# Performance work log

Hardware: AMD Instinct MI355X
Metric: run time of the kernel (lower is better)

## Reference

```python
import jax, jax.numpy as jnp
import numpy as np

BN, S, D = 200, 128, 1024          # B*N entity rows, scenes, d_model
D_INNER, D_STATE, D_CONV = 2048, 32, 4


def setup_inputs() -> dict:
    key = jax.random.key(0)
    ks = jax.random.split(key, 8)
    s = 0.02
    return {
        "x": jax.random.normal(ks[0], (BN, S, D), jnp.float32),
        "emotion_bias": jax.random.uniform(ks[1], (BN, S, 1), jnp.float32),
        "norm_w": jnp.ones((D,), jnp.float32),
        "norm_b": jnp.zeros((D,), jnp.float32),
        "in_proj_W": jax.random.normal(ks[2], (2 * D_INNER, D), jnp.float32) * s,
        "conv_w": jax.random.normal(ks[3], (D_INNER, 1, D_CONV), jnp.float32) * 0.1,
        "conv_b": jnp.zeros((D_INNER,), jnp.float32),
        "x_proj_W": jax.random.normal(ks[4], (2 * D_STATE + 1, D_INNER), jnp.float32) * s,
        "dt_W": jax.random.normal(ks[5], (D_INNER, 1), jnp.float32),
        "dt_b": jnp.zeros((D_INNER,), jnp.float32),
        "out_W": jax.random.normal(ks[6], (D, D_INNER), jnp.float32) * s,
        "emotion_scale": jnp.array(0.1, jnp.float32),
    }


def reference(x, emotion_bias, norm_w, norm_b, in_proj_W, conv_w, conv_b,
              x_proj_W, dt_W, dt_b, out_W, emotion_scale):
    residual = x
    # LayerNorm (eps=1e-5, biased variance as in torch)
    mu = x.mean(-1, keepdims=True)
    var = ((x - mu) ** 2).mean(-1, keepdims=True)
    xn = (x - mu) * jax.lax.rsqrt(var + 1e-5) * norm_w + norm_b

    xz = xn @ in_proj_W.T                      # [BN, S, 2*d_inner]
    x_in, z = jnp.split(xz, 2, axis=-1)

    # causal depthwise conv1d (torch pads d_conv-1 both sides, truncates to S == left-pad only)
    xc = jax.lax.conv_general_dilated(
        x_in.transpose(0, 2, 1), conv_w,
        window_strides=(1,), padding=[(D_CONV - 1, 0)],
        feature_group_count=D_INNER,
        dimension_numbers=("NCH", "OIH", "NCH"))
    xc = (xc + conv_b[None, :, None]).transpose(0, 2, 1)   # [BN, S, d_inner]
    x_act = jax.nn.silu(xc)

    x_ssm = x_act @ x_proj_W.T                 # [BN, S, 2*d_state+1]
    delta_raw, B_mat, C = jnp.split(x_ssm, [1, 1 + D_STATE], axis=-1)
    delta = jax.nn.softplus(delta_raw @ dt_W.T + dt_b)     # [BN, S, d_inner]
    delta = jnp.maximum(delta + emotion_scale * emotion_bias, 1e-4)

    def step(h, inp):
        d_t, B_t, C_t, xa_t = inp              # [BN,d_inner],[BN,n],[BN,n],[BN,d_inner]
        h = h * jnp.exp(-d_t)[..., None] + B_t[:, None, :] * xa_t[..., None]
        h = jnp.clip(h, -100.0, 100.0)
        y_t = jnp.einsum("bdn,bn->bd", h, C_t)
        return h, y_t

    h0 = jnp.zeros((BN, D_INNER, D_STATE), jnp.float32)
    xs = (delta.transpose(1, 0, 2), B_mat.transpose(1, 0, 2),
          C.transpose(1, 0, 2), x_act.transpose(1, 0, 2))
    _, y = jax.lax.scan(step, h0, xs)          # y: [S, BN, d_inner]
    y = y.transpose(1, 0, 2)

    return (y * jax.nn.silu(z)) @ out_W.T + residual
```

## Files before the change

kernel.cpp:

```cpp
#include <hip/hip_runtime.h>
#include <cstdint>
#include <cstddef>

#define NBN   200
#define NS    128
#define ND    1024
#define NDI   2048
#define NST   32
#define NROWS (NBN * NS)

typedef __attribute__((ext_vector_type(8))) short bf16x8;
typedef __attribute__((ext_vector_type(4))) float f32x4;

__device__ __forceinline__ unsigned short f2bf(float f) {
    unsigned int u = __float_as_uint(f);
    u += 0x7fffu + ((u >> 16) & 1u);
    return (unsigned short)(u >> 16);
}
__device__ __forceinline__ float bf2f(unsigned short h) {
    return __uint_as_float(((unsigned int)h) << 16);
}

__device__ __forceinline__ void gl_lds16(const void* g, void* l) {
    typedef __attribute__((address_space(1))) const unsigned int* gp_t;
    typedef __attribute__((address_space(3))) unsigned int* lp_t;
    __builtin_amdgcn_global_load_lds((gp_t)(uintptr_t)g,
                                     (lp_t)(unsigned int)(uintptr_t)l, 16, 0, 0);
}

__global__ __launch_bounds__(256) void cvt_kernel(const float* __restrict__ src,
                                                  unsigned short* __restrict__ dst, int n) {
    int i = blockIdx.x * 256 + threadIdx.x;
    if (i < n) dst[i] = f2bf(src[i]);
}

__global__ __launch_bounds__(256) void padwx_kernel(const float* __restrict__ src,
                                                    unsigned short* __restrict__ dst) {
    int i = blockIdx.x * 256 + threadIdx.x;
    int r = i >> 11;
    dst[i] = (r < 65) ? f2bf(src[i]) : (unsigned short)0;
}

__global__ __launch_bounds__(256) void ln_kernel(const float* __restrict__ x,
                                                 const float* __restrict__ gw,
                                                 const float* __restrict__ gb,
                                                 unsigned short* __restrict__ xn) {
    __shared__ float ss[4], ss2[4];
    size_t row = blockIdx.x;
    int tid = threadIdx.x;
    const float4* px = (const float4*)(x + row * ND);
    float4 v = px[tid];
    float s  = v.x + v.y + v.z + v.w;
    float s2 = fmaf(v.x, v.x, fmaf(v.y, v.y, fmaf(v.z, v.z, v.w * v.w)));
    #pragma unroll
    for (int off = 32; off > 0; off >>= 1) {
        s  += __shfl_down(s,  off, 64);
        s2 += __shfl_down(s2, off, 64);
    }
    if ((tid & 63) == 0) { ss[tid >> 6] = s; ss2[tid >> 6] = s2; }
    __syncthreads();
    float tot  = ss[0] + ss[1] + ss[2] + ss[3];
    float tot2 = ss2[0] + ss2[1] + ss2[2] + ss2[3];
    float mu   = tot * (1.f / ND);
    float var  = fmaf(tot2, 1.f / ND, -mu * mu);
    float rstd = rsqrtf(var + 1e-5f);
    float4 wv = ((const float4*)gw)[tid];
    float4 bv = ((const float4*)gb)[tid];
    ushort4 o;
    o.x = f2bf(fmaf((v.x - mu) * rstd, wv.x, bv.x));
    o.y = f2bf(fmaf((v.y - mu) * rstd, wv.y, bv.y));
    o.z = f2bf(fmaf((v.z - mu) * rstd, wv.z, bv.z));
    o.w = f2bf(fmaf((v.w - mu) * rstd, wv.w, bv.w));
    ((ushort4*)(xn + row * ND))[tid] = o;
}

template <int EPI>
__global__ __launch_bounds__(256, 2)
void gemm_bt128(const unsigned short* __restrict__ A,
                const unsigned short* __restrict__ B,
                int K, int N,
                void* __restrict__ outp,
                const float* __restrict__ resid) {
    __shared__ __align__(16) unsigned short As[128 * 32];
    __shared__ __align__(16) unsigned short Bs[128 * 32];
    const int tid  = threadIdx.x;
    const int bm   = blockIdx.x;
    const int bn   = blockIdx.y;
    const int wid  = tid >> 6;
    const int lane = tid & 63;
    const int wm   = (wid >> 1) * 64;
    const int wn   = (wid & 1) * 64;
    const int lrow = lane & 15;
    const int kq   = lane >> 4;

    f32x4 acc[4][4];
    #pragma unroll
    for (int i = 0; i < 4; i++)
        #pragma unroll
        for (int j = 0; j < 4; j++) acc[i][j] = (f32x4){0.f, 0.f, 0.f, 0.f};

    const size_t a_row0 = (size_t)bm * 128;
    const size_t b_row0 = (size_t)bn * 128;

    const int r1 = tid >> 2;
    const int c8 = (tid & 3) << 3;
    const unsigned short* gA1 = A + (a_row0 + r1) * K + c8;
    const unsigned short* gA2 = A + (a_row0 + 64 + r1) * K + c8;
    const unsigned short* gB1 = B + (b_row0 + r1) * K + c8;
    const unsigned short* gB2 = B + (b_row0 + 64 + r1) * K + c8;
    char* lA1 = (char*)As + wid * 1024;
    char* lA2 = (char*)As + wid * 1024 + 4096;
    char* lB1 = (char*)Bs + wid * 1024;
    char* lB2 = (char*)Bs + wid * 1024 + 4096;

    for (int kt = 0; kt < K; kt += 32) {
        __syncthreads();
        gl_lds16(gA1, lA1); gl_lds16(gA2, lA2);
        gl_lds16(gB1, lB1); gl_lds16(gB2, lB2);
        gA1 += 32; gA2 += 32; gB1 += 32; gB2 += 32;
        __syncthreads();
        bf16x8 af[4], bfr[4];
        #pragma unroll
        for (int mi = 0; mi < 4; mi++)
            af[mi] = *(const bf16x8*)&As[(wm + mi * 16 + lrow) * 32 + kq * 8];
        #pragma unroll
        for (int ni = 0; ni < 4; ni++)
            bfr[ni] = *(const bf16x8*)&Bs[(wn + ni * 16 + lrow) * 32 + kq * 8];
        #pragma unroll
        for (int mi = 0; mi < 4; mi++)
            #pragma unroll
            for (int ni = 0; ni < 4; ni++)
                acc[mi][ni] = __builtin_amdgcn_mfma_f32_16x16x32_bf16(af[mi], bfr[ni], acc[mi][ni], 0, 0, 0);
    }

    #pragma unroll
    for (int mi = 0; mi < 4; mi++)
        #pragma unroll
        for (int ni = 0; ni < 4; ni++)
            #pragma unroll
            for (int r = 0; r < 4; r++) {
                size_t row = a_row0 + wm + mi * 16 + kq * 4 + r;
                size_t col = b_row0 + wn + ni * 16 + lrow;
                float v = acc[mi][ni][r];
                size_t idx = row * (size_t)N + col;
                if (EPI == 0) ((unsigned short*)outp)[idx] = f2bf(v);
                else          ((float*)outp)[idx] = v + resid[idx];
            }
}

__global__ __launch_bounds__(256) void conv_silu_kernel(const unsigned short* __restrict__ xz,
                                                        const float* __restrict__ cw,
                                                        const float* __restrict__ cb,
                                                        unsigned short* __restrict__ xact) {
    int tid = blockIdx.x * 256 + threadIdx.x;
    int c = tid & (NDI - 1);
    int b = tid >> 11;
    float4 wv = ((const float4*)cw)[c];
    float w0 = wv.x, w1 = wv.y, w2 = wv.z, w3 = wv.w;
    float bias = cb[c];
    const unsigned short* px = xz + (size_t)b * NS * (2 * NDI) + c;
    unsigned short* po = xact + (size_t)b * NS * NDI + c;
    float x0 = 0.f, x1 = 0.f, x2 = 0.f;
    for (int t = 0; t < NS; t++) {
        float x3 = bf2f(px[(size_t)t * (2 * NDI)]);
        float v  = fmaf(x3, w3, fmaf(x2, w2, fmaf(x1, w1, fmaf(x0, w0, bias))));
        float s  = v * __builtin_amdgcn_rcpf(1.f + __expf(-v));
        po[(size_t)t * NDI] = f2bf(s);
        x0 = x1; x1 = x2; x2 = x3;
    }
}

__global__ __launch_bounds__(256, 2)
void gemm2_kernel(const unsigned short* __restrict__ A,
                  const unsigned short* __restrict__ B,
                  float* __restrict__ out) {
    __shared__ __align__(16) unsigned short As[64 * 32];
    __shared__ __align__(16) unsigned short Bs[80 * 32];
    const int tid  = threadIdx.x;
    const int bm   = blockIdx.x;
    const int wid  = tid >> 6;
    const int lane = tid & 63;
    const int lrow = lane & 15;
    const int kq   = lane >> 4;

    f32x4 acc[5];
    #pragma unroll
    for (int i = 0; i < 5; i++) acc[i] = (f32x4){0.f, 0.f, 0.f, 0.f};

    const int r1 = tid >> 2;
    const int c8 = (tid & 3) << 3;
    const unsigned short* gA1 = A + ((size_t)bm * 64 + r1) * NDI + c8;
    const unsigned short* gB1 = B + (size_t)r1 * NDI + c8;
    const unsigned short* gB2 = B + (size_t)(64 + r1) * NDI + c8;
    char* lA1 = (char*)As + wid * 1024;
    char* lB1 = (char*)Bs + wid * 1024;
    char* lB2 = (char*)Bs + 4096;

    for (int kt = 0; kt < NDI; kt += 32) {
        __syncthreads();
        gl_lds16(gA1, lA1);
        gl_lds16(gB1, lB1);
        if (tid < 64) gl_lds16(gB2, lB2);
        gA1 += 32; gB1 += 32; gB2 += 32;
        __syncthreads();
        bf16x8 af = *(const bf16x8*)&As[(wid * 16 + lrow) * 32 + kq * 8];
        #pragma unroll
        for (int ni = 0; ni < 5; ni++) {
            bf16x8 bfr = *(const bf16x8*)&Bs[(ni * 16 + lrow) * 32 + kq * 8];
            acc[ni] = __builtin_amdgcn_mfma_f32_16x16x32_bf16(af, bfr, acc[ni], 0, 0, 0);
        }
    }
    #pragma unroll
    for (int ni = 0; ni < 5; ni++)
        #pragma unroll
        for (int r = 0; r < 4; r++) {
            size_t row = (size_t)bm * 64 + wid * 16 + kq * 4 + r;
            int col = ni * 16 + lrow;
            out[row * 80 + col] = acc[ni][r];
        }
}

__global__ __launch_bounds__(256)
void scan_kernel(const float* __restrict__ xssm,
                 unsigned short* xact_g,
                 const unsigned short* __restrict__ xz,
                 const float* __restrict__ dtW,
                 const float* __restrict__ dtb,
                 const float* __restrict__ eb,
                 const float* __restrict__ es_p) {
    __shared__ __align__(16) float sB[NS][NST];
    __shared__ __align__(16) float sC[NS][NST];
    __shared__ float sDR[NS];
    __shared__ float sDE[NS];
    const int tid = threadIdx.x;
    const int b   = blockIdx.y;
    const int d   = blockIdx.x * 256 + tid;

    for (int i = tid; i < NS * 65; i += 256) {
        int t = i / 65, c = i - t * 65;
        float v = xssm[((size_t)b * NS + t) * 80 + c];
        if (c == 0)      sDR[t] = v;
        else if (c < 33) sB[t][c - 1] = v;
        else             sC[t][c - 33] = v;
    }
    {
        float es = es_p[0];
        for (int i = tid; i < NS; i += 256) sDE[i] = es * eb[b * NS + i];
    }
    __syncthreads();

    const float w  = dtW[d];
    const float bb = dtb[d];
    float h[NST];
    #pragma unroll
    for (int n = 0; n < NST; n++) h[n] = 0.f;

    unsigned short* p        = xact_g + (size_t)b * NS * NDI + d;
    const unsigned short* pz = xz + (size_t)b * NS * (2 * NDI) + NDI + d;

    for (int t = 0; t < NS; t++) {
        float xa = bf2f(*p);
        float zz = bf2f(*pz);
        float raw = fmaf(sDR[t], w, bb);
        float sp  = (raw > 20.f) ? raw : __logf(1.f + __expf(raw));
        float delta = fmaxf(sp + sDE[t], 1e-4f);
        float a = __expf(-delta);
        float y = 0.f;
        #pragma unroll
        for (int n8 = 0; n8 < 8; n8++) {
            f32x4 Bv = *(const f32x4*)&sB[t][n8 * 4];
            f32x4 Cv = *(const f32x4*)&sC[t][n8 * 4];
            #pragma unroll
            for (int j = 0; j < 4; j++) {
                h[n8 * 4 + j] = fmaf(h[n8 * 4 + j], a, Bv[j] * xa);
                y = fmaf(h[n8 * 4 + j], Cv[j], y);
            }
        }
        float sig = __builtin_amdgcn_rcpf(1.f + __expf(-zz));
        *p = f2bf(y * zz * sig);
        p += NDI; pz += 2 * NDI;
    }
}

extern "C" void kernel_launch(void* const* d_in, const int* in_sizes, int n_in,
                              void* d_out, int out_size, void* d_ws, size_t ws_size,
                              hipStream_t stream) {
    const float* x   = (const float*)d_in[0];
    const float* eb  = (const float*)d_in[1];
    const float* nw  = (const float*)d_in[2];
    const float* nb  = (const float*)d_in[3];
    const float* Wi  = (const float*)d_in[4];
    const float* cw  = (const float*)d_in[5];
    const float* cb  = (const float*)d_in[6];
    const float* Wx  = (const float*)d_in[7];
    const float* dtW = (const float*)d_in[8];
    const float* dtb = (const float*)d_in[9];
    const float* Wo  = (const float*)d_in[10];
    const float* es  = (const float*)d_in[11];
    float* out = (float*)d_out;

    char* ws = (char*)d_ws;
    unsigned short* wi_b   = (unsigned short*)(ws + 0);
    unsigned short* wo_b   = (unsigned short*)(ws + 8388608);
    unsigned short* wx_b   = (unsigned short*)(ws + 12582912);
    unsigned short* xz_b   = (unsigned short*)(ws + 12910592);
    unsigned short* xact_b = (unsigned short*)(ws + 222625792);
    float*          xssm   = (float*)(ws + 327483392);
    if (ws_size < (size_t)335675392) return;

    cvt_kernel<<<(2 * NDI * ND + 255) / 256, 256, 0, stream>>>(Wi, wi_b, 2 * NDI * ND);
    cvt_kernel<<<(ND * NDI + 255) / 256, 256, 0, stream>>>(Wo, wo_b, ND * NDI);
    padwx_kernel<<<(80 * NDI) / 256, 256, 0, stream>>>(Wx, wx_b);

    unsigned short* xn_b = xact_b;
    ln_kernel<<<NROWS, 256, 0, stream>>>(x, nw, nb, xn_b);

    gemm_bt128<0><<<dim3(NROWS / 128, (2 * NDI) / 128), 256, 0, stream>>>(
        xn_b, wi_b, ND, 2 * NDI, xz_b, nullptr);

    conv_silu_kernel<<<(NBN * NDI) / 256, 256, 0, stream>>>(xz_b, cw, cb, xact_b);

    gemm2_kernel<<<NROWS / 64, 256, 0, stream>>>(xact_b, wx_b, xssm);

    scan_kernel<<<dim3(NDI / 256, NBN), 256, 0, stream>>>(xssm, xact_b, xz_b, dtW, dtb, eb, es);

    gemm_bt128<1><<<dim3(NROWS / 128, ND / 128), 256, 0, stream>>>(
        xact_b, wo_b, NDI, ND, out, x);
}
```

Before: 965.2 us.

## Replace 128x128 GEMM with pipelined 256x256 tile kernel with LDS swizzle

After: 960.7 us. About the same (-0.5%).

```diff
diff --git a/kernel.cpp b/kernel.cpp
--- a/kernel.cpp
+++ b/kernel.cpp
@@ -74,75 +74,129 @@
     ((ushort4*)(xn + row * ND))[tid] = o;
 }
 
-template <int EPI>
-__global__ __launch_bounds__(256, 2)
-void gemm_bt128(const unsigned short* __restrict__ A,
-                const unsigned short* __restrict__ B,
-                int K, int N,
-                void* __restrict__ outp,
-                const float* __restrict__ resid) {
-    __shared__ __align__(16) unsigned short As[128 * 32];
-    __shared__ __align__(16) unsigned short Bs[128 * 32];
+
+#define BARRIER __builtin_amdgcn_s_barrier()
+#define LGKM0  asm volatile("s_waitcnt lgkmcnt(0)" ::: "memory")
+#define VMCNT6 asm volatile("s_waitcnt vmcnt(6)" ::: "memory")
+#define VMCNT0 asm volatile("s_waitcnt vmcnt(0)" ::: "memory")
+#define NOWAIT ((void)0)
+#define PRIO1  __builtin_amdgcn_s_setprio(1)
+#define PRIO0  __builtin_amdgcn_s_setprio(0)
+
+#define STG_A(t, kp) {                                                        \
+    gl_lds16(gA0 + (size_t)(t) * 64 + (kp) * 32,                              \
+             lA + (((t) & 1) << 15) + ((kp) << 14));                          \
+    gl_lds16(gA1 + (size_t)(t) * 64 + (kp) * 32,                              \
+             lA + (((t) & 1) << 15) + ((kp) << 14) + 8192); }
+#define STG_B(t, kp) {                                                        \
+    gl_lds16(gB0 + (size_t)(t) * 64 + (kp) * 32,                              \
+             lB + (((t) & 1) << 15) + ((kp) << 14));                          \
+    gl_lds16(gB1 + (size_t)(t) * 64 + (kp) * 32,                              \
+             lB + (((t) & 1) << 15) + ((kp) << 14) + 8192); }
+
+#define RD_A(dst, mh, kp) { _Pragma("unroll")                                 \
+    for (int mi = 0; mi < 4; ++mi)                                            \
+        dst[mi] = *(const bf16x8*)(aRd + bo + (kp) * 16384 + (mh) * 4096 + mi * 1024); }
+#define RD_B(dst, kp) { _Pragma("unroll")                                     \
+    for (int ni = 0; ni < 4; ++ni)                                            \
+        dst[ni] = *(const bf16x8*)(bRd + bo + (kp) * 16384 + ni * 1024); }
+
+#define MM(mh, AV, BV) { _Pragma("unroll")                                    \
+    for (int mi = 0; mi < 4; ++mi) { _Pragma("unroll")                        \
+        for (int ni = 0; ni < 4; ++ni)                                        \
+            acc[(mh) * 4 + mi][ni] = __builtin_amdgcn_mfma_f32_16x16x32_bf16( \
+                AV[mi], BV[ni], acc[(mh) * 4 + mi][ni], 0, 0, 0); } }
+
+#define TILE(t, DO_AP1, DO_T2, W) {                                           \
+    const int bo = ((t) & 1) << 15;                                           \
+                                                          \
+    RD_A(aK0, 0, 0); RD_B(bK0, 0);                                            \
+    if (DO_AP1) STG_A((t) + 1, 1);                                            \
+    BARRIER; LGKM0; PRIO1; MM(0, aK0, bK0); PRIO0; BARRIER;                   \
+                                                          \
+    RD_A(aK1, 0, 1); RD_B(bK1, 1);                                            \
+    if (DO_T2) STG_B((t) + 2, 0);                                             \
+    BARRIER; LGKM0; PRIO1; MM(0, aK1, bK1); PRIO0; BARRIER;                   \
+                                                          \
+    RD_A(aK0, 1, 0);                                                          \
+    if (DO_T2) STG_B((t) + 2, 1);                                             \
+    BARRIER; LGKM0; PRIO1; MM(1, aK0, bK0); PRIO0; BARRIER;                   \
+                                                          \
+    RD_A(aK1, 1, 1);                                                          \
+    if (DO_T2) STG_A((t) + 2, 0);                                             \
+    BARRIER; LGKM0; PRIO1; MM(1, aK1, bK1); PRIO0;                            \
+    W;                                                                        \
+    BARRIER; }
+
+template <int K, int EPI>
+__global__ __launch_bounds__(512, 2)
+void gemm256(const unsigned short* __restrict__ A,
+             const unsigned short* __restrict__ B,
+             int N, void* __restrict__ outp, const float* __restrict__ resid) {
+    constexpr int NT = K / 64;
+    static_assert(NT >= 3, "need >=3 K-tiles");
+    __shared__ __align__(16) char smem[131072];
+
     const int tid  = threadIdx.x;
-    const int bm   = blockIdx.x;
-    const int bn   = blockIdx.y;
+    const int lane = tid & 63;
     const int wid  = tid >> 6;
-    const int lane = tid & 63;
-    const int wm   = (wid >> 1) * 64;
-    const int wn   = (wid & 1) * 64;
     const int lrow = lane & 15;
     const int kq   = lane >> 4;
-
-    f32x4 acc[4][4];
-    #pragma unroll
-    for (int i = 0; i < 4; i++)
-        #pragma unroll
-        for (int j = 0; j < 4; j++) acc[i][j] = (f32x4){0.f, 0.f, 0.f, 0.f};
-
-    const size_t a_row0 = (size_t)bm * 128;
-    const size_t b_row0 = (size_t)bn * 128;
-
-    const int r1 = tid >> 2;
-    const int c8 = (tid & 3) << 3;
-    const unsigned short* gA1 = A + (a_row0 + r1) * K + c8;
-    const unsigned short* gA2 = A + (a_row0 + 64 + r1) * K + c8;
-    const unsigned short* gB1 = B + (b_row0 + r1) * K + c8;
-    const unsigned short* gB2 = B + (b_row0 + 64 + r1) * K + c8;
-    char* lA1 = (char*)As + wid * 1024;
-    char* lA2 = (char*)As + wid * 1024 + 4096;
-    char* lB1 = (char*)Bs + wid * 1024;
-    char* lB2 = (char*)Bs + wid * 1024 + 4096;
-
-    for (int kt = 0; kt < K; kt += 32) {
-        __syncthreads();
-        gl_lds16(gA1, lA1); gl_lds16(gA2, lA2);
-        gl_lds16(gB1, lB1); gl_lds16(gB2, lB2);
-        gA1 += 32; gA2 += 32; gB1 += 32; gB2 += 32;
-        __syncthreads();
-        bf16x8 af[4], bfr[4];
-        #pragma unroll
-        for (int mi = 0; mi < 4; mi++)
-            af[mi] = *(const bf16x8*)&As[(wm + mi * 16 + lrow) * 32 + kq * 8];
-        #pragma unroll
-        for (int ni = 0; ni < 4; ni++)
-            bfr[ni] = *(const bf16x8*)&Bs[(wn + ni * 16 + lrow) * 32 + kq * 8];
-        #pragma unroll
-        for (int mi = 0; mi < 4; mi++)
+    const int wmi  = wid >> 2;
+    const int wni  = wid & 3;
+
+    const int gx  = gridDim.x;
+    const int nwg = gx * gridDim.y;
+    const int lin = blockIdx.y * gx + blockIdx.x;
+    const int id2 = (lin & 7) * (nwg >> 3) + (lin >> 3);
+    const int bm  = id2 % gx;
+    const int bn  = id2 / gx;
+
+    const size_t m0 = (size_t)bm * 256;
+    const size_t n0 = (size_t)bn * 256;
+
+    const int fr = (lrow >> 1) & 3;
+    const char* aRd = smem +          (wmi * 128 + lrow) * 64 + ((kq ^ fr) << 4);
+    const char* bRd = smem + 65536 + (wni * 64  + lrow) * 64 + ((kq ^ fr) << 4);
+
+    const int srow = wid * 16 + (lane >> 2);
+    const int scol = (((lane & 3) ^ ((lane >> 3) & 3)) << 3);
+    const unsigned short* gA0 = A + (m0 + srow) * K + scol;
+    const unsigned short* gA1 = A + (m0 + 128 + srow) * K + scol;
+    const unsigned short* gB0 = B + (n0 + srow) * K + scol;
+    const unsigned short* gB1 = B + (n0 + 128 + srow) * K + scol;
+    char* lA = smem + wid * 1024;
+    char* lB = smem + 65536 + wid * 1024;
+
+    f32x4 acc[8][4];
+    #pragma unroll
+    for (int i = 0; i < 8; ++i)
+        #pragma unroll
+        for (int j = 0; j < 4; ++j) acc[i][j] = (f32x4){0.f, 0.f, 0.f, 0.f};
+
+    bf16x8 aK0[4], aK1[4], bK0[4], bK1[4];
+
+    STG_B(0, 0); STG_B(0, 1); STG_A(0, 0); STG_A(0, 1);
+    STG_B(1, 0); STG_B(1, 1); STG_A(1, 0);
+    VMCNT6;
+    BARRIER;
+
+    int t = 0;
+    #pragma unroll 2
+    for (; t < NT - 2; ++t) { TILE(t, 1, 1, VMCNT6); }
+    TILE((NT - 2), 1, 0, VMCNT0);
+    TILE((NT - 1), 0, 0, NOWAIT);
+
+    #pragma unroll
+    for (int mi = 0; mi < 8; ++mi)
+        #pragma unroll
+        for (int ni = 0; ni < 4; ++ni)
             #pragma unroll
-            for (int ni = 0; ni < 4; ni++)
-                acc[mi][ni] = __builtin_amdgcn_mfma_f32_16x16x32_bf16(af[mi], bfr[ni], acc[mi][ni], 0, 0, 0);
-    }
-
-    #pragma unroll
-    for (int mi = 0; mi < 4; mi++)
-        #pragma unroll
-        for (int ni = 0; ni < 4; ni++)
-            #pragma unroll
-            for (int r = 0; r < 4; r++) {
-                size_t row = a_row0 + wm + mi * 16 + kq * 4 + r;
-                size_t col = b_row0 + wn + ni * 16 + lrow;
+            for (int r = 0; r < 4; ++r) {
+                size_t row = m0 + wmi * 128 + mi * 16 + kq * 4 + r;
+                size_t col = n0 + wni * 64 + ni * 16 + lrow;
+                size_t idx = row * (size_t)N + col;
                 float v = acc[mi][ni][r];
-                size_t idx = row * (size_t)N + col;
                 if (EPI == 0) ((unsigned short*)outp)[idx] = f2bf(v);
                 else          ((float*)outp)[idx] = v + resid[idx];
             }
@@ -315,8 +369,8 @@
     unsigned short* xn_b = xact_b;
     ln_kernel<<<NROWS, 256, 0, stream>>>(x, nw, nb, xn_b);
 
-    gemm_bt128<0><<<dim3(NROWS / 128, (2 * NDI) / 128), 256, 0, stream>>>(
-        xn_b, wi_b, ND, 2 * NDI, xz_b, nullptr);
+    gemm256<ND, 0><<<dim3(NROWS / 256, (2 * NDI) / 256), 512, 0, stream>>>(
+        xn_b, wi_b, 2 * NDI, xz_b, nullptr);
 
     conv_silu_kernel<<<(NBN * NDI) / 256, 256, 0, stream>>>(xz_b, cw, cb, xact_b);
 
@@ -324,6 +378,6 @@
 
     scan_kernel<<<dim3(NDI / 256, NBN), 256, 0, stream>>>(xssm, xact_b, xz_b, dtW, dtb, eb, es);
 
-    gemm_bt128<1><<<dim3(NROWS / 128, ND / 128), 256, 0, stream>>>(
-        xact_b, wo_b, NDI, ND, out, x);
-}
+    gemm256<NDI, 1><<<dim3(NROWS / 256, ND / 256), 512, 0, stream>>>(
+        xact_b, wo_b, ND, out, x);
+}
```
